# Kernel optimization log

Hardware: AMD Instinct MI355X
Metric: run time of the kernel (lower is better)

Reference implementation:

```python
import jax, jax.numpy as jnp
import numpy as np

NPOINT = 2048
RADIUS = 0.4
NSAMPLE = 32
BN_EPS = 1e-5


def setup_inputs() -> dict:
    key = jax.random.key(0)
    ks = jax.random.split(key, 6)
    B, N, C = 8, 8192, 64
    xyz = jax.random.normal(ks[0], (B, N, 3), jnp.float32)
    points = jax.random.normal(ks[1], (B, N, C), jnp.float32)
    W1 = jax.random.normal(ks[2], (3 + C, 64), jnp.float32) * 0.1
    W2 = jax.random.normal(ks[3], (64, 64), jnp.float32) * 0.1
    W3 = jax.random.normal(ks[4], (64, 128), jnp.float32) * 0.1
    return dict(
        xyz=xyz, points=points,
        W1=W1, g1=jnp.ones(64), b1=jnp.zeros(64),
        W2=W2, g2=jnp.ones(64), b2=jnp.zeros(64),
        W3=W3, g3=jnp.ones(128), b3=jnp.zeros(128),
    )


def _furthest_point_sample(xyz, npoint):
    # xyz: (B, N, 3) -> (B, npoint) int32. Sequential max-min scan, batched.
    B, N, _ = xyz.shape

    def step(carry, _):
        dists, last = carry
        p = jnp.take_along_axis(xyz, last[:, None, None], axis=1)  # (B,1,3)
        d2 = jnp.sum((xyz - p) ** 2, axis=-1)                       # (B,N)
        dists = jnp.minimum(dists, d2)
        nxt = jnp.argmax(dists, axis=-1).astype(jnp.int32)
        return (dists, nxt), nxt

    init = (jnp.full((B, N), 1e10, xyz.dtype), jnp.zeros((B,), jnp.int32))
    _, idx = jax.lax.scan(step, init, None, length=npoint - 1)      # (npoint-1, B)
    idx = jnp.concatenate([jnp.zeros((1, B), jnp.int32), idx], axis=0)
    return idx.T                                                    # (B, npoint)


def _ball_query(xyz, new_xyz, radius, nsample):
    # For each centroid take the first nsample point indices (in original order)
    # within `radius`; pad with the first found index (CUDA ball_query semantics).
    B, N, _ = xyz.shape
    d2 = jnp.sum((new_xyz[:, :, None, :] - xyz[:, None, :, :]) ** 2, axis=-1)  # (B,S,N)
    mask = d2 < radius * radius
    key = jnp.where(mask, jnp.arange(N, dtype=jnp.int32), N)
    srt = jnp.sort(key, axis=-1)[..., :nsample]                     # (B,S,K)
    first = srt[..., :1]
    first = jnp.where(first == N, 0, first)                         # empty ball -> index 0
    return jnp.where(srt == N, first, srt)


def _gather(pts, idx):
    # pts: (B,N,D), idx: (B,...) -> (B,...,D)
    return jax.vmap(lambda p, i: p[i])(pts, idx)


def reference(xyz, points, W1, g1, b1, W2, g2, b2, W3, g3, b3):
    fps_idx = _furthest_point_sample(xyz, NPOINT)                   # (B,S)
    new_xyz = _gather(xyz, fps_idx)                                 # (B,S,3)
    idx = _ball_query(xyz, new_xyz, RADIUS, NSAMPLE)                # (B,S,K)
    grouped_xyz = _gather(xyz, idx) - new_xyz[:, :, None, :]        # (B,S,K,3)
    grouped_pts = _gather(points, idx)                              # (B,S,K,C)
    feats = jnp.concatenate([grouped_xyz, grouped_pts], axis=-1)    # (B,S,K,3+C)
    for W, g, b in ((W1, g1, b1), (W2, g2, b2), (W3, g3, b3)):
        feats = feats @ W                                           # 1x1 conv
        m = feats.mean(axis=(0, 1, 2))
        v = feats.var(axis=(0, 1, 2))                               # biased, torch BN train mode
        feats = g * (feats - m) * jax.lax.rsqrt(v + BN_EPS) + b
        feats = jax.nn.relu(feats)
    new_points = feats.max(axis=2)                                  # max over nsample -> (B,S,mlp[-1])
    return new_xyz, new_points
```

## Files before the change

kernel.cpp:

```cpp
#include <hip/hip_runtime.h>

constexpr int B_ = 8, N_ = 8192, NPOINT_ = 2048, NSAMPLE_ = 32;
constexpr int M_ROWS = B_ * NPOINT_ * NSAMPLE_;
constexpr int NGROUP = B_ * NPOINT_;
constexpr size_t OFF_NXF   = 0;
constexpr size_t OFF_IDX   = 196608;
constexpr size_t OFF_WF    = 1245184;
constexpr size_t OFF_GB    = 1311488;
constexpr size_t OFF_STATS = 1313536;
constexpr size_t OFF_NP    = 1315584;
constexpr size_t OFF_FLAG  = 1317632;
constexpr size_t OFF_MAXB  = 2097152;

__device__ __forceinline__ float bf2f(unsigned short u) {
  union { unsigned u; float f; } x; x.u = ((unsigned)u) << 16; return x.f;
}
__device__ __forceinline__ float lo16f(unsigned u) {
  union { unsigned u; float f; } x; x.u = u << 16; return x.f;
}
__device__ __forceinline__ float hi16f(unsigned u) {
  union { unsigned u; float f; } x; x.u = u & 0xffff0000u; return x.f;
}
__device__ __forceinline__ unsigned short f2bf(float f) {
  union { float f; unsigned u; } x; x.f = f;
  unsigned u = x.u + 0x7FFFu + ((x.u >> 16) & 1u);
  return (unsigned short)(u >> 16);
}
__device__ __forceinline__ void unpack8(uint4 u, float* x) {
  x[0] = bf2f((unsigned short)(u.x & 0xffffu)); x[1] = bf2f((unsigned short)(u.x >> 16));
  x[2] = bf2f((unsigned short)(u.y & 0xffffu)); x[3] = bf2f((unsigned short)(u.y >> 16));
  x[4] = bf2f((unsigned short)(u.z & 0xffffu)); x[5] = bf2f((unsigned short)(u.z >> 16));
  x[6] = bf2f((unsigned short)(u.w & 0xffffu)); x[7] = bf2f((unsigned short)(u.w >> 16));
}
__device__ __forceinline__ float ldf(const void* p, size_t i, bool bf) {
  return bf ? bf2f(((const unsigned short*)p)[i]) : ((const float*)p)[i];
}
__device__ __forceinline__ void stf(void* p, size_t i, bool bf, float v) {
  if (bf) ((unsigned short*)p)[i] = f2bf(v);
  else    ((float*)p)[i] = v;
}

extern "C" __global__ void detect_kernel(const unsigned short* __restrict__ xyz,
                                         int* __restrict__ flag) {
  if (threadIdx.x == 0 && blockIdx.x == 0) {
    int sane = 0;
    for (int k = 0; k < 32; ++k) {
      int e = (xyz[2 * k] >> 7) & 0xff;
      if (e >= 90 && e <= 140) ++sane;
    }
    *flag = (sane >= 24) ? 1 : 0;
  }
}

extern "C" __global__ void prep_kernel(
    const void* W1, const void* W2, const void* W3,
    const void* g1, const void* b1, const void* g2, const void* b2,
    const void* g3, const void* b3,
    float* __restrict__ wf, float* __restrict__ gb, const int* __restrict__ flag) {
  const bool bf = (*flag != 0);
  int i = blockIdx.x * 256 + threadIdx.x;
  if (i < 4288)       wf[i] = ldf(W1, i, bf);
  else if (i < 8384)  wf[i] = ldf(W2, i - 4288, bf);
  else if (i < 16576) wf[i] = ldf(W3, i - 8384, bf);
  else if (i < 17088) {
    int k = i - 16576; float v;
    if (k < 64)       v = ldf(g1, k, bf);
    else if (k < 128) v = ldf(b1, k - 64, bf);
    else if (k < 192) v = ldf(g2, k - 128, bf);
    else if (k < 256) v = ldf(b2, k - 192, bf);
    else if (k < 384) v = ldf(g3, k - 256, bf);
    else              v = ldf(b3, k - 384, bf);
    gb[k] = v;
  }
}

template <bool BF>
__device__ __forceinline__ void fps_body(
    const void* xyz, void* out, float* __restrict__ nxf,
    unsigned short* sxyz, float (*sv)[16], int (*si)[16]) {
#pragma clang fp contract(off)
  const int b = blockIdx.x;
  const int t = threadIdx.x;
  const int lane = t & 63, w = t >> 6;
  const size_t base = (size_t)b * N_ * 3;
  unsigned cc[12];
  float px[8], py[8], pz[8];
  float d[8];
  if (BF) {
    const uint4* xp = (const uint4*)((const unsigned short*)xyz + base) + t * 3;
    uint4* sp = (uint4*)sxyz + t * 3;
#pragma unroll
    for (int m = 0; m < 3; ++m) {
      uint4 u = xp[m];
      sp[m] = u;
      cc[4*m+0] = u.x; cc[4*m+1] = u.y; cc[4*m+2] = u.z; cc[4*m+3] = u.w;
    }
  } else {
#pragma unroll
    for (int k = 0; k < 8; ++k) {
      int i = t * 8 + k;
      px[k] = ((const float*)xyz)[base + i*3 + 0];
      py[k] = ((const float*)xyz)[base + i*3 + 1];
      pz[k] = ((const float*)xyz)[base + i*3 + 2];
    }
  }
#pragma unroll
  for (int k = 0; k < 8; ++k) d[k] = 1e10f;
  __syncthreads();
  float s0x=0.f,s0y=0.f,s0z=0.f, s1x=0.f,s1y=0.f,s1z=0.f;
  float p0, p1, p2;
  if (BF) { p0 = bf2f(sxyz[0]); p1 = bf2f(sxyz[1]); p2 = bf2f(sxyz[2]); }
  else {
    p0 = ((const float*)xyz)[base + 0];
    p1 = ((const float*)xyz)[base + 1];
    p2 = ((const float*)xyz)[base + 2];
  }
  if (t == 0) { s0x = p0; s0y = p1; s0z = p2; }
  for (int j = 1; j < NPOINT_; ++j) {
    float bv = -1.0f; int bk = 0;
#pragma unroll
    for (int k = 0; k < 8; ++k) {
      float x, y, z;
      if (BF) {
        if ((k & 1) == 0) {
          unsigned ra = cc[(3*k) >> 1], rb = cc[((3*k) >> 1) + 1];
          x = lo16f(ra); y = hi16f(ra); z = lo16f(rb);
        } else {
          unsigned ra = cc[(3*k - 1) >> 1], rb = cc[(3*k + 1) >> 1];
          x = hi16f(ra); y = lo16f(rb); z = hi16f(rb);
        }
      } else { x = px[k]; y = py[k]; z = pz[k]; }
      float dx = x - p0, dy = y - p1, dz = z - p2;
      float d2 = (dx*dx + dy*dy) + dz*dz;
      float dn = fminf(d[k], d2);
      d[k] = dn;
      if (dn > bv) { bv = dn; bk = k; }
    }
    float bv0 = bv;
#pragma unroll
    for (int off = 1; off < 64; off <<= 1)
      bv = fmaxf(bv, __shfl_xor(bv, off));
    unsigned long long m = __ballot(bv0 == bv);
    int sl = (int)__builtin_ctzll(m);
    int pi = __shfl(t * 8 + bk, sl);
    const int pb = j & 1;
    if (lane == 0) { sv[pb][w] = bv; si[pb][w] = pi; }
    __syncthreads();
    float gv = sv[pb][0]; int gpi = si[pb][0];
#pragma unroll
    for (int q = 1; q < 16; ++q) {
      float v2 = sv[pb][q]; int i2 = si[pb][q];
      if (v2 > gv) { gv = v2; gpi = i2; }
    }
    if (BF) {
      int wo3 = gpi * 3;
      p0 = bf2f(sxyz[wo3 + 0]); p1 = bf2f(sxyz[wo3 + 1]); p2 = bf2f(sxyz[wo3 + 2]);
    } else {
      size_t wo = base + (size_t)gpi * 3;
      p0 = ((const float*)xyz)[wo + 0];
      p1 = ((const float*)xyz)[wo + 1];
      p2 = ((const float*)xyz)[wo + 2];
    }
    if (t == (j & 1023)) {
      if ((j >> 10) == 0) { s0x = p0; s0y = p1; s0z = p2; }
      else                { s1x = p0; s1y = p1; s1z = p2; }
    }
  }
  const bool bfrt = BF;
#pragma unroll
  for (int s = 0; s < 2; ++s) {
    float cx = (s==0)?s0x:s1x;
    float cy = (s==0)?s0y:s1y;
    float cz = (s==0)?s0z:s1z;
    size_t o = ((size_t)b * NPOINT_ + s * 1024 + t) * 3;
    nxf[o+0] = cx; nxf[o+1] = cy; nxf[o+2] = cz;
    stf(out, o+0, bfrt, cx); stf(out, o+1, bfrt, cy); stf(out, o+2, bfrt, cz);
  }
}

extern "C" __global__ void __launch_bounds__(1024, 4) fps_kernel(
    const void* xyz, void* out, float* __restrict__ nxf,
    const int* __restrict__ flag) {
  __shared__ unsigned short sxyz[N_ * 3];
  __shared__ float sv[2][16];
  __shared__ int   si[2][16];
  if (*flag != 0) fps_body<true>(xyz, out, nxf, sxyz, sv, si);
  else            fps_body<false>(xyz, out, nxf, sxyz, sv, si);
}

extern "C" __global__ void __launch_bounds__(256) ballq_kernel(
    const void* xyz, const float* __restrict__ nxf,
    unsigned short* __restrict__ idxout, const int* __restrict__ flag) {
#pragma clang fp contract(off)
  const bool bf = (*flag != 0);
  const int gw = (int)((blockIdx.x * 256 + threadIdx.x) >> 6);
  const int lane = threadIdx.x & 63;
  const int b = gw >> 11;
  const int j = gw & (NPOINT_ - 1);
  const size_t base = (size_t)b * N_ * 3;
  const size_t co = ((size_t)b * NPOINT_ + j) * 3;
  const float c0 = nxf[co], c1 = nxf[co+1], c2 = nxf[co+2];
  unsigned short* out = idxout + (size_t)gw * NSAMPLE_;
  int cnt = 0, first = 0;
  for (int c = 0; c < N_/64 && cnt < NSAMPLE_; ++c) {
    int i = c * 64 + lane;
    float x = ldf(xyz, base + i*3 + 0, bf);
    float y = ldf(xyz, base + i*3 + 1, bf);
    float z = ldf(xyz, base + i*3 + 2, bf);
    float dx = x - c0, dy = y - c1, dz = z - c2;
    float d2 = (dx*dx + dy*dy) + dz*dz;
    unsigned long long m = __ballot(d2 < 0.16f);
    if (lane == 0) {
      while (m && cnt < NSAMPLE_) {
        int bit = __builtin_ctzll(m);
        int pi = c * 64 + bit;
        if (cnt == 0) first = pi;
        out[cnt] = (unsigned short)pi;
        ++cnt;
        m &= (m - 1);
      }
    }
    cnt = __shfl(cnt, 0);
  }
  first = __shfl(first, 0);
  if (lane >= cnt && lane < NSAMPLE_) out[lane] = (unsigned short)first;
}

__device__ __forceinline__ void l1_row(
    const void* xyz, const void* points, const float* __restrict__ nxf,
    const unsigned short* __restrict__ idx, const float* __restrict__ wf,
    int r, bool bf, float* acc) {
  const int b = r >> 16;
  const int j = (r >> 5) & (NPOINT_ - 1);
  const int i = idx[r];
  const size_t pt = (size_t)b * N_ + i;
  const float* cp = nxf + ((size_t)b * NPOINT_ + j) * 3;
  float f0 = ldf(xyz, pt*3 + 0, bf) - cp[0];
  float f1 = ldf(xyz, pt*3 + 1, bf) - cp[1];
  float f2 = ldf(xyz, pt*3 + 2, bf) - cp[2];
#pragma unroll
  for (int c = 0; c < 64; ++c)
    acc[c] = fmaf(f0, wf[c], fmaf(f1, wf[64+c], f2 * wf[128+c]));
  const float* wp = wf + 192;
  if (bf) {
    const uint4* pp = (const uint4*)((const unsigned short*)points + pt * 64);
#pragma unroll
    for (int s = 0; s < 8; ++s) {
      uint4 u = pp[s];
      float x[8]; unpack8(u, x);
#pragma unroll
      for (int kk = 0; kk < 8; ++kk)
#pragma unroll
        for (int c = 0; c < 64; ++c)
          acc[c] = fmaf(x[kk], wp[(s*8+kk)*64 + c], acc[c]);
    }
  } else {
    const float4* pp = (const float4*)((const float*)points + pt * 64);
#pragma unroll
    for (int s = 0; s < 16; ++s) {
      float4 u = pp[s];
      float x[4] = {u.x, u.y, u.z, u.w};
#pragma unroll
      for (int kk = 0; kk < 4; ++kk)
#pragma unroll
        for (int c = 0; c < 64; ++c)
          acc[c] = fmaf(x[kk], wp[(s*4+kk)*64 + c], acc[c]);
    }
  }
}

template <int LDW>
__device__ __forceinline__ void mm64(const float* v, const float* __restrict__ w,
                                     float* acc) {
#pragma unroll
  for (int ch = 0; ch < 64; ++ch)
#pragma unroll
    for (int c = 0; c < 64; ++c)
      acc[c] = fmaf(v[ch], w[ch*LDW + c], acc[c]);
}

__device__ __forceinline__ void bnrelu64(float* v, const float* __restrict__ np0) {
#pragma unroll
  for (int c = 0; c < 64; ++c)
    v[c] = fmaxf(fmaf(v[c], np0[c], np0[64 + c]), 0.f);
}

__device__ __forceinline__ void commit_stats64(float* a, float* __restrict__ stats) {
  float q[64];
#pragma unroll
  for (int c = 0; c < 64; ++c) q[c] = a[c] * a[c];
#pragma unroll
  for (int off = 1; off < 64; off <<= 1)
#pragma unroll
    for (int c = 0; c < 64; ++c) {
      a[c] += __shfl_xor(a[c], off);
      q[c] += __shfl_xor(q[c], off);
    }
  __shared__ float LS[4][64], LQ[4][64];
  const int t = threadIdx.x, w = t >> 6;
  if ((t & 63) == 0) {
#pragma unroll
    for (int c = 0; c < 64; ++c) { LS[w][c] = a[c]; LQ[w][c] = q[c]; }
  }
  __syncthreads();
  if (t < 64) {
    atomicAdd(&stats[t],      LS[0][t] + LS[1][t] + LS[2][t] + LS[3][t]);
    atomicAdd(&stats[64 + t], LQ[0][t] + LQ[1][t] + LQ[2][t] + LQ[3][t]);
  }
}

extern "C" __global__ void __launch_bounds__(256) p1_kernel(
    const void* xyz, const void* points, const float* __restrict__ nxf,
    const unsigned short* __restrict__ idx, const float* __restrict__ wf,
    float* __restrict__ stats, const int* __restrict__ flag) {
  const bool bf = (*flag != 0);
  const int r = blockIdx.x * 256 + threadIdx.x;
  float acc[64];
  l1_row(xyz, points, nxf, idx, wf, r, bf, acc);
  commit_stats64(acc, stats);
}

extern "C" __global__ void __launch_bounds__(256, 2) p2_kernel(
    const void* xyz, const void* points, const float* __restrict__ nxf,
    const unsigned short* __restrict__ idx, const float* __restrict__ wf,
    const float* __restrict__ w2, const float* __restrict__ np1,
    float* __restrict__ stats, const int* __restrict__ flag) {
  const bool bf = (*flag != 0);
  const int r = blockIdx.x * 256 + threadIdx.x;
  float v[64];
  l1_row(xyz, points, nxf, idx, wf, r, bf, v);
  bnrelu64(v, np1);
  float acc[64];
#pragma unroll
  for (int c = 0; c < 64; ++c) acc[c] = 0.f;
  mm64<64>(v, w2, acc);
  commit_stats64(acc, stats);
}

extern "C" __global__ void __launch_bounds__(256, 2) p3_kernel(
    const void* xyz, const void* points, const float* __restrict__ nxf,
    const unsigned short* __restrict__ idx, const float* __restrict__ wf,
    const float* __restrict__ w2, const float* __restrict__ w3,
    const float* __restrict__ np1, const float* __restrict__ np2,
    unsigned short* __restrict__ maxb, float* __restrict__ stats,
    const int* __restrict__ flag) {
  const bool bf = (*flag != 0);
  const int t = threadIdx.x, lane = t & 63, w = t >> 6;
  const int h = __builtin_amdgcn_readfirstlane(w & 1);
  const int g = blockIdx.x * 4 + (w >> 1) * 2 + (lane >> 5);
  const int r = g * 32 + (lane & 31);
  float v[64];
  l1_row(xyz, points, nxf, idx, wf, r, bf, v);
  bnrelu64(v, np1);
  float y2[64];
#pragma unroll
  for (int c = 0; c < 64; ++c) y2[c] = 0.f;
  mm64<64>(v, w2, y2);
  bnrelu64(y2, np2);
  const float* w3h = w3 + h * 64;
  float y3[64];
#pragma unroll
  for (int c = 0; c < 64; ++c) y3[c] = 0.f;
  mm64<128>(y2, w3h, y3);
  float* s = v; float* q = y2;
#pragma unroll
  for (int c = 0; c < 64; ++c) { s[c] = y3[c]; q[c] = y3[c] * y3[c]; }
#pragma unroll
  for (int off = 1; off <= 16; off <<= 1)
#pragma unroll
    for (int c = 0; c < 64; ++c)
      y3[c] = fmaxf(y3[c], __shfl_xor(y3[c], off));
  if ((lane & 31) == 0) {
    unsigned short* mo = maxb + (size_t)g * 128 + h * 64;
#pragma unroll
    for (int c = 0; c < 64; ++c) mo[c] = f2bf(y3[c]);
  }
#pragma unroll
  for (int off = 1; off < 64; off <<= 1)
#pragma unroll
    for (int c = 0; c < 64; ++c) {
      s[c] += __shfl_xor(s[c], off);
      q[c] += __shfl_xor(q[c], off);
    }
  __shared__ float LS[4][64], LQ[4][64];
  if (lane == 0) {
#pragma unroll
    for (int c = 0; c < 64; ++c) { LS[w][c] = s[c]; LQ[w][c] = q[c]; }
  }
  __syncthreads();
  if (t < 128) {
    int hh = t >> 6, cl = t & 63;
    atomicAdd(&stats[t],       LS[hh][cl] + LS[hh+2][cl]);
    atomicAdd(&stats[128 + t], LQ[hh][cl] + LQ[hh+2][cl]);
  }
}

extern "C" __global__ void nparam_kernel(
    const float* __restrict__ stats, const float* __restrict__ g,
    const float* __restrict__ bb, float* __restrict__ npar, int Cc) {
  int c = threadIdx.x;
  if (c < Cc) {
    float m = stats[c] * (1.0f / M_ROWS);
    float v = stats[Cc + c] * (1.0f / M_ROWS) - m * m;
    float sc = g[c] / sqrtf(v + 1e-5f);
    npar[c] = sc;
    npar[Cc + c] = bb[c] - m * sc;
  }
}

extern "C" __global__ void __launch_bounds__(256) final_kernel(
    const unsigned short* __restrict__ maxb, const float* __restrict__ npar,
    void* out, const int* __restrict__ flag) {
  const bool bf = (*flag != 0);
  const int gtid = blockIdx.x * 256 + threadIdx.x;
  const int c = gtid & 127;
  float y = bf2f(maxb[gtid]);
  float r = fmaxf(fmaf(y, npar[c], npar[128 + c]), 0.f);
  stf(out, (size_t)B_ * NPOINT_ * 3 + gtid, bf, r);
}

extern "C" void kernel_launch(void* const* d_in, const int* in_sizes, int n_in,
                              void* d_out, int out_size, void* d_ws, size_t ws_size,
                              hipStream_t stream) {
  const void* xyz    = d_in[0];
  const void* points = d_in[1];
  char* ws = (char*)d_ws;
  float* nxf   = (float*)(ws + OFF_NXF);
  unsigned short* wsIdx = (unsigned short*)(ws + OFF_IDX);
  float* wf    = (float*)(ws + OFF_WF);
  float* gb    = (float*)(ws + OFF_GB);
  float* stats = (float*)(ws + OFF_STATS);
  float* npar  = (float*)(ws + OFF_NP);
  int*   flag  = (int*)(ws + OFF_FLAG);
  unsigned short* maxb = (unsigned short*)(ws + OFF_MAXB);

  hipMemsetAsync(stats, 0, 512 * sizeof(float), stream);
  detect_kernel<<<1, 64, 0, stream>>>((const unsigned short*)xyz, flag);
  prep_kernel<<<67, 256, 0, stream>>>(d_in[2], d_in[5], d_in[8], d_in[3], d_in[4],
                                      d_in[6], d_in[7], d_in[9], d_in[10], wf, gb, flag);
  fps_kernel<<<B_, 1024, 0, stream>>>(xyz, d_out, nxf, flag);
  ballq_kernel<<<(B_ * NPOINT_) / 4, 256, 0, stream>>>(xyz, nxf, wsIdx, flag);
  p1_kernel<<<M_ROWS / 256, 256, 0, stream>>>(xyz, points, nxf, wsIdx, wf, stats, flag);
  nparam_kernel<<<1, 128, 0, stream>>>(stats, gb, gb + 64, npar, 64);
  p2_kernel<<<M_ROWS / 256, 256, 0, stream>>>(xyz, points, nxf, wsIdx, wf, wf + 4288,
                                              npar, stats + 128, flag);
  nparam_kernel<<<1, 128, 0, stream>>>(stats + 128, gb + 128, gb + 192, npar + 128, 64);
  p3_kernel<<<(2 * M_ROWS) / 256, 256, 0, stream>>>(xyz, points, nxf, wsIdx, wf,
                                                    wf + 4288, wf + 8384, npar,
                                                    npar + 128, maxb, stats + 256, flag);
  nparam_kernel<<<1, 128, 0, stream>>>(stats + 256, gb + 256, gb + 384, npar + 256, 128);
  final_kernel<<<(NGROUP * 128) / 256, 256, 0, stream>>>(maxb, npar + 256, d_out, flag);
}
```

Before: 4.235 ms.

## Use packed 64-bit LDS atomicMax for FPS cross-wave argmax reduction

Replaces the per-wave shared arrays and the 16-way serial scan after the barrier with one packed (distance bits, inverted index) 64-bit atomicMax into a rotating triple of LDS slots. The slots rotate so that each iteration needs only one barrier. It also pre-unpacks the bf16 coordinates into float registers once, and finds the argmax index only in lanes that hold the wave maximum rather than tracking it on every compare. Possible costs are LDS atomic contention from 16 waves and slightly higher register use. Tie-breaking still favours the lowest index through the inverted index bits.

```diff
diff --git a/kernel.cpp b/kernel.cpp
--- a/kernel.cpp
+++ b/kernel.cpp
@@ -25,6 +25,9 @@
   union { float f; unsigned u; } x; x.f = f;
   unsigned u = x.u + 0x7FFFu + ((x.u >> 16) & 1u);
   return (unsigned short)(u >> 16);
+}
+__device__ __forceinline__ unsigned f2u(float f) {
+  union { float f; unsigned u; } x; x.f = f; return x.u;
 }
 __device__ __forceinline__ void unpack8(uint4 u, float* x) {
   x[0] = bf2f((unsigned short)(u.x & 0xffffu)); x[1] = bf2f((unsigned short)(u.x >> 16));
@@ -77,23 +80,32 @@
 template <bool BF>
 __device__ __forceinline__ void fps_body(
     const void* xyz, void* out, float* __restrict__ nxf,
-    unsigned short* sxyz, float (*sv)[16], int (*si)[16]) {
+    unsigned short* sxyz, unsigned long long* slots) {
 #pragma clang fp contract(off)
   const int b = blockIdx.x;
   const int t = threadIdx.x;
-  const int lane = t & 63, w = t >> 6;
+  const int lane = t & 63;
   const size_t base = (size_t)b * N_ * 3;
-  unsigned cc[12];
-  float px[8], py[8], pz[8];
-  float d[8];
+  float px[8], py[8], pz[8], d[8];
   if (BF) {
     const uint4* xp = (const uint4*)((const unsigned short*)xyz + base) + t * 3;
     uint4* sp = (uint4*)sxyz + t * 3;
+    unsigned cc[12];
 #pragma unroll
     for (int m = 0; m < 3; ++m) {
       uint4 u = xp[m];
       sp[m] = u;
       cc[4*m+0] = u.x; cc[4*m+1] = u.y; cc[4*m+2] = u.z; cc[4*m+3] = u.w;
+    }
+#pragma unroll
+    for (int k = 0; k < 8; ++k) {
+      if ((k & 1) == 0) {
+        unsigned ra = cc[(3*k) >> 1], rb = cc[((3*k) >> 1) + 1];
+        px[k] = lo16f(ra); py[k] = hi16f(ra); pz[k] = lo16f(rb);
+      } else {
+        unsigned ra = cc[(3*k - 1) >> 1], rb = cc[(3*k + 1) >> 1];
+        px[k] = hi16f(ra); py[k] = lo16f(rb); pz[k] = hi16f(rb);
+      }
     }
   } else {
 #pragma unroll
@@ -106,6 +118,7 @@
   }
 #pragma unroll
   for (int k = 0; k < 8; ++k) d[k] = 1e10f;
+  if (t < 3) slots[t] = 0ull;
   __syncthreads();
   float s0x=0.f,s0y=0.f,s0z=0.f, s1x=0.f,s1y=0.f,s1z=0.f;
   float p0, p1, p2;
@@ -117,41 +130,39 @@
   }
   if (t == 0) { s0x = p0; s0y = p1; s0z = p2; }
   for (int j = 1; j < NPOINT_; ++j) {
-    float bv = -1.0f; int bk = 0;
+    float bv = -1.0f;
 #pragma unroll
     for (int k = 0; k < 8; ++k) {
-      float x, y, z;
-      if (BF) {
-        if ((k & 1) == 0) {
-          unsigned ra = cc[(3*k) >> 1], rb = cc[((3*k) >> 1) + 1];
-          x = lo16f(ra); y = hi16f(ra); z = lo16f(rb);
-        } else {
-          unsigned ra = cc[(3*k - 1) >> 1], rb = cc[(3*k + 1) >> 1];
-          x = hi16f(ra); y = lo16f(rb); z = hi16f(rb);
-        }
-      } else { x = px[k]; y = py[k]; z = pz[k]; }
-      float dx = x - p0, dy = y - p1, dz = z - p2;
+      float dx = px[k] - p0, dy = py[k] - p1, dz = pz[k] - p2;
       float d2 = (dx*dx + dy*dy) + dz*dz;
       float dn = fminf(d[k], d2);
       d[k] = dn;
-      if (dn > bv) { bv = dn; bk = k; }
+      bv = fmaxf(bv, dn);
     }
     float bv0 = bv;
 #pragma unroll
     for (int off = 1; off < 64; off <<= 1)
       bv = fmaxf(bv, __shfl_xor(bv, off));
-    unsigned long long m = __ballot(bv0 == bv);
+    int bk = 0;
+    bool hit = (bv0 == bv);
+    if (hit) {
+#pragma unroll
+      for (int k = 7; k >= 0; --k)
+        if (d[k] == bv0) bk = k;
+    }
+    unsigned long long m = __ballot(hit);
     int sl = (int)__builtin_ctzll(m);
     int pi = __shfl(t * 8 + bk, sl);
-    const int pb = j & 1;
-    if (lane == 0) { sv[pb][w] = bv; si[pb][w] = pi; }
+    const int ss = j % 3;
+    if (lane == 0) {
+      unsigned long long key =
+          ((unsigned long long)f2u(bv) << 32) | (unsigned)(~pi);
+      atomicMax(&slots[ss], key);
+    }
+    if (t == 0) slots[(ss + 1) % 3] = 0ull;
     __syncthreads();
-    float gv = sv[pb][0]; int gpi = si[pb][0];
-#pragma unroll
-    for (int q = 1; q < 16; ++q) {
-      float v2 = sv[pb][q]; int i2 = si[pb][q];
-      if (v2 > gv) { gv = v2; gpi = i2; }
-    }
+    unsigned long long key2 = slots[ss];
+    int gpi = (int)(~(unsigned)key2);
     if (BF) {
       int wo3 = gpi * 3;
       p0 = bf2f(sxyz[wo3 + 0]); p1 = bf2f(sxyz[wo3 + 1]); p2 = bf2f(sxyz[wo3 + 2]);
@@ -182,10 +193,9 @@
     const void* xyz, void* out, float* __restrict__ nxf,
     const int* __restrict__ flag) {
   __shared__ unsigned short sxyz[N_ * 3];
-  __shared__ float sv[2][16];
-  __shared__ int   si[2][16];
-  if (*flag != 0) fps_body<true>(xyz, out, nxf, sxyz, sv, si);
-  else            fps_body<false>(xyz, out, nxf, sxyz, sv, si);
+  __shared__ unsigned long long slots[3];
+  if (*flag != 0) fps_body<true>(xyz, out, nxf, sxyz, slots);
+  else            fps_body<false>(xyz, out, nxf, sxyz, slots);
 }
 
 extern "C" __global__ void __launch_bounds__(256) ballq_kernel(
```

New measurement: 3.822 ms. 9.7% less time.
